# Kernel tuning notes

Measured on AMD Instinct MI355X. Metric: run time of the kernel, lower is better.

Reference implementation:

```python
import jax, jax.numpy as jnp
import numpy as np

N_WORDS, MAX_CHARS = 16384, 16
CE, H1, WE, H2 = 32, 64, 64, 128
CHAR_VOCAB, WORD_VOCAB, N_TAGS = 128, 50257, 64


def setup_inputs() -> dict:
    key = jax.random.key(0)
    ks = jax.random.split(key, 16)
    f = lambda k, shape: (jax.random.normal(k, shape, dtype=jnp.float32) * 0.1)
    return {
        "char_ids": jax.random.randint(ks[0], (N_WORDS, MAX_CHARS), 0, CHAR_VOCAB, dtype=jnp.int32),
        "word_ids": jax.random.randint(ks[1], (N_WORDS,), 0, WORD_VOCAB, dtype=jnp.int32),
        "char_lens": jax.random.randint(ks[2], (N_WORDS,), 1, MAX_CHARS + 1, dtype=jnp.int32),
        "char_emb": f(ks[3], (CHAR_VOCAB, CE)),
        "word_emb": f(ks[4], (WORD_VOCAB, WE)),
        "Wih1": f(ks[5], (4 * H1, CE)), "Whh1": f(ks[6], (4 * H1, H1)),
        "bih1": f(ks[7], (4 * H1,)), "bhh1": f(ks[8], (4 * H1,)),
        "Wih2": f(ks[9], (4 * H2, WE + H1)), "Whh2": f(ks[10], (4 * H2, H2)),
        "bih2": f(ks[11], (4 * H2,)), "bhh2": f(ks[12], (4 * H2,)),
        "Wtag": f(ks[13], (N_TAGS, H2)), "btag": f(ks[14], (N_TAGS,)),
    }


def _gates(pre, c, h_dim):
    i, fg, g, o = jnp.split(pre, 4, axis=-1)  # PyTorch LSTM gate order: i,f,g,o
    c_new = jax.nn.sigmoid(fg) * c + jax.nn.sigmoid(i) * jnp.tanh(g)
    h_new = jax.nn.sigmoid(o) * jnp.tanh(c_new)
    return h_new, c_new


def reference(char_ids, word_ids, char_lens, char_emb, word_emb,
              Wih1, Whh1, bih1, bhh1, Wih2, Whh2, bih2, bhh2, Wtag, btag):
    n_words, max_chars = char_ids.shape
    # ---- char LSTM, batched over all words, zero init per word ----
    cx = char_emb[char_ids]                      # [N, T, CE]
    cx = jnp.transpose(cx, (1, 0, 2))            # [T, N, CE]
    valid = (jnp.arange(max_chars)[:, None] < char_lens[None, :])  # [T, N]
    b1 = bih1 + bhh1

    def char_step(carry, inp):
        h, c = carry
        x, v = inp
        pre = x @ Wih1.T + h @ Whh1.T + b1
        h_new, c_new = _gates(pre, c, H1)
        v = v[:, None]
        return (jnp.where(v, h_new, h), jnp.where(v, c_new, c)), None

    h0 = jnp.zeros((n_words, Wih1.shape[0] // 4), cx.dtype)
    (h_char, _), _ = jax.lax.scan(char_step, (h0, h0), (cx, valid))  # h at true length

    # ---- word LSTM, sequential over words (hidden2 carried across) ----
    wx = jnp.concatenate([word_emb[word_ids], h_char], axis=-1)  # [N, WE+H1]
    b2 = bih2 + bhh2

    def word_step(carry, x):
        h, c = carry
        pre = x @ Wih2.T + h @ Whh2.T + b2
        h_new, c_new = _gates(pre, c, H2)
        return (h_new, c_new), h_new

    h20 = jnp.zeros((Wih2.shape[0] // 4,), wx.dtype)
    _, hs = jax.lax.scan(word_step, (h20, h20), wx)  # [N, H2]

    logits = hs @ Wtag.T + btag
    return jax.nn.log_softmax(logits, axis=1)
```

## Files before the change

### kernel.cpp

```cpp
#include <hip/hip_runtime.h>
#include <math.h>

#define N_WORDS 16384
#define MAX_CHARS 16
#define CE 32
#define H1 64
#define WE 64
#define H2 128
#define N_TAGS 64

typedef _Float16 f16x8 __attribute__((ext_vector_type(8)));
typedef float f32x4 __attribute__((ext_vector_type(4)));
typedef int i32x8 __attribute__((ext_vector_type(8)));

__device__ __forceinline__ float rcpf(float x) { return __builtin_amdgcn_rcpf(x); }
__device__ __forceinline__ float sigf(float x) { return rcpf(1.0f + __expf(-x)); }
__device__ __forceinline__ float tanh2(float x) {
    return 1.f - 2.f * rcpf(__expf(2.f * x) + 1.f);
}

extern "C" __global__ void __launch_bounds__(1024)
char_lstm_kernel(const int* __restrict__ char_ids, const int* __restrict__ char_lens,
                 const float* __restrict__ char_emb,
                 const float* __restrict__ Wih1, const float* __restrict__ Whh1,
                 const float* __restrict__ bih1, const float* __restrict__ bhh1,
                 float* __restrict__ h_char)
{
    extern __shared__ float lds[];
    float* Wc = lds;
    float* b1 = Wc + 256 * 97;
    float* xh = b1 + 256;
    const int tid = threadIdx.x;

    for (int idx = tid; idx < 256 * 96; idx += 1024) {
        int r = idx / 96, k = idx - r * 96;
        float v = (k < CE) ? Wih1[r * CE + k] : Whh1[r * H1 + (k - CE)];
        Wc[r * 97 + k] = v;
    }
    for (int r = tid; r < 256; r += 1024) b1[r] = bih1[r] + bhh1[r];
    __syncthreads();

    const int wlocal = tid >> 6;
    const int lane   = tid & 63;
    const int word   = blockIdx.x * 16 + wlocal;
    const int len    = char_lens[word];
    float h = 0.f, c = 0.f;
    float* xhw = xh + wlocal * 97;

    for (int t = 0; t < MAX_CHARS; ++t) {
        int cid = char_ids[word * MAX_CHARS + t];
        if (lane < CE) xhw[lane] = char_emb[cid * CE + lane];
        xhw[CE + lane] = h;
        __syncthreads();

        float a0 = 0.f, a1 = 0.f, a2 = 0.f, a3 = 0.f;
        const float* w0 = Wc + (0 * 64 + lane) * 97;
        const float* w1 = Wc + (1 * 64 + lane) * 97;
        const float* w2 = Wc + (2 * 64 + lane) * 97;
        const float* w3 = Wc + (3 * 64 + lane) * 97;
        #pragma unroll 8
        for (int k = 0; k < 96; ++k) {
            float x = xhw[k];
            a0 += w0[k] * x; a1 += w1[k] * x; a2 += w2[k] * x; a3 += w3[k] * x;
        }
        float pi = a0 + b1[lane];
        float pf = a1 + b1[64 + lane];
        float pg = a2 + b1[128 + lane];
        float po = a3 + b1[192 + lane];
        if (t < len) {
            float ig = sigf(pi), fg = sigf(pf), gg = tanh2(pg), og = sigf(po);
            c = fg * c + ig * gg;
            h = og * tanh2(c);
        }
        __syncthreads();
    }
    h_char[word * H1 + lane] = h;
}

extern "C" __global__ void __launch_bounds__(256)
xpre_gemm_kernel(const int* __restrict__ word_ids, const float* __restrict__ word_emb,
                 const float* __restrict__ h_char,
                 const float* __restrict__ Wih2,
                 const float* __restrict__ bih2, const float* __restrict__ bhh2,
                 float* __restrict__ xpre)
{
    __shared__ float Wl[64 * 130];
    __shared__ float Xl[32 * 130];
    const int tid = threadIdx.x;
    const int wb = blockIdx.x * 32;
    const int cb = blockIdx.y * 64;

    for (int idx = tid; idx < 64 * 128; idx += 256) {
        int r = idx >> 7, k = idx & 127;
        Wl[r * 130 + k] = Wih2[(cb + r) * H2 + k];
    }
    for (int idx = tid; idx < 32 * 128; idx += 256) {
        int w = idx >> 7, k = idx & 127;
        float v = (k < WE) ? word_emb[(long)word_ids[wb + w] * WE + k]
                           : h_char[(long)(wb + w) * H1 + (k - WE)];
        Xl[w * 130 + k] = v;
    }
    __syncthreads();

    const int tc = tid & 31;
    const int wg = tid >> 5;
    float acc[4][2] = {};
    for (int k = 0; k < 128; ++k) {
        float wv0 = Wl[tc * 130 + k];
        float wv1 = Wl[(tc + 32) * 130 + k];
        #pragma unroll
        for (int i = 0; i < 4; ++i) {
            float x = Xl[(wg * 4 + i) * 130 + k];
            acc[i][0] += x * wv0;
            acc[i][1] += x * wv1;
        }
    }
    int c0 = cb + tc, c1 = cb + tc + 32;
    float b0 = bih2[c0] + bhh2[c0];
    float b1v = bih2[c1] + bhh2[c1];
    int o0 = (c0 & 127) * 4 + (c0 >> 7);
    int o1 = (c1 & 127) * 4 + (c1 >> 7);
    #pragma unroll
    for (int i = 0; i < 4; ++i) {
        long w = wb + wg * 4 + i;
        xpre[w * 512 + o0] = acc[i][0] + b0;
        xpre[w * 512 + o1] = acc[i][1] + b1v;
    }
}

extern "C" __global__ void __launch_bounds__(512)
word_lstm_kernel(const float* __restrict__ xpre, const float* __restrict__ Whh2,
                 float* __restrict__ hs)
{
    __shared__ __align__(16) unsigned char h8[2][128];
    const int tid = threadIdx.x;
    const int w   = tid >> 6;
    const int l   = tid & 63;
    const int lg  = l >> 4;
    const int lc  = l & 15;
    const int hidx = 16 * w + lc;
    const bool writer = (l < 16);

    i32x8 af8[4];
    #pragma unroll
    for (int g = 0; g < 4; ++g) {
        const float* wrow = Whh2 + (size_t)(g * 128 + hidx) * 128 + lg * 32;
        i32x8 a;
        #pragma unroll
        for (int r = 0; r < 8; ++r) {
            int pk = __builtin_amdgcn_cvt_pk_fp8_f32(wrow[r * 4 + 0], wrow[r * 4 + 1], 0, false);
            pk = __builtin_amdgcn_cvt_pk_fp8_f32(wrow[r * 4 + 2], wrow[r * 4 + 3], pk, true);
            a[r] = pk;
        }
        af8[g] = a;
    }
    if (tid < 128) h8[0][tid] = 0;
    float c = 0.f;
    float4 xp = *(const float4*)(xpre + hidx * 4);
    float hbuf[8];
    const f32x4 zf = {0.f, 0.f, 0.f, 0.f};
    __syncthreads();

    for (int t8 = 0; t8 < N_WORDS / 8; ++t8) {
        #pragma unroll
        for (int j = 0; j < 8; ++j) {
            const int t = t8 * 8 + j;
            const int tn = (t + 1) & (N_WORDS - 1);
            float4 xpn = *(const float4*)(xpre + (size_t)tn * 512 + hidx * 4);

            const unsigned char* hb = h8[j & 1] + lg * 32;
            i32x8 bf = *(const i32x8*)hb;

            f32x4 acc[4];
            #pragma unroll
            for (int g = 0; g < 4; ++g)
                acc[g] = __builtin_amdgcn_mfma_scale_f32_16x16x128_f8f6f4(
                    bf, af8[g], zf, 0, 0, 0, 0x7F7F7F7F, 0, 0x7F7F7F7F);

            float p0 = acc[0][0] + xp.x;
            float p1 = acc[1][0] + xp.y;
            float p2 = acc[2][0] + xp.z;
            float p3 = acc[3][0] + xp.w;
            float ig = sigf(p0), fg = sigf(p1);
            float gg = tanh2(p2), og = sigf(p3);
            c = fg * c + ig * gg;
            float hn = og * tanh2(c);
            hbuf[j] = hn;
            if (writer) {
                int hp = __builtin_amdgcn_cvt_pk_fp8_f32(hn, hn, 0, false);
                h8[(j + 1) & 1][hidx] = (unsigned char)hp;
            }
            xp = xpn;

            asm volatile("s_waitcnt lgkmcnt(0)" ::: "memory");
            __builtin_amdgcn_sched_barrier(0);
            __builtin_amdgcn_s_barrier();
            __builtin_amdgcn_sched_barrier(0);
        }
        if (writer) {
            #pragma unroll
            for (int jj = 0; jj < 8; ++jj)
                hs[(size_t)(t8 * 8 + jj) * 128 + hidx] = hbuf[jj];
        }
    }
}

extern "C" __global__ void __launch_bounds__(256)
tag_kernel(const float* __restrict__ hs, const float* __restrict__ Wtag,
           const float* __restrict__ btag, float* __restrict__ out)
{
    __shared__ float Wl[64 * 129];
    const int tid = threadIdx.x;
    for (int idx = tid; idx < 64 * 128; idx += 256) {
        int r = idx >> 7, k = idx & 127;
        Wl[r * 129 + k] = Wtag[r * H2 + k];
    }
    __syncthreads();

    const int lane = tid & 63;
    const int word = blockIdx.x * 4 + (tid >> 6);
    const float* hrow = hs + (long)word * H2;
    float acc = btag[lane];
    #pragma unroll 4
    for (int k = 0; k < 128; ++k) acc += Wl[lane * 129 + k] * hrow[k];

    float m = acc;
    #pragma unroll
    for (int off = 32; off > 0; off >>= 1) m = fmaxf(m, __shfl_xor(m, off));
    float e = expf(acc - m);
    float s = e;
    #pragma unroll
    for (int off = 32; off > 0; off >>= 1) s += __shfl_xor(s, off);
    out[(long)word * N_TAGS + lane] = acc - m - logf(s);
}

extern "C" void kernel_launch(void* const* d_in, const int* in_sizes, int n_in,
                              void* d_out, int out_size, void* d_ws, size_t ws_size,
                              hipStream_t stream)
{
    (void)in_sizes; (void)n_in; (void)out_size; (void)ws_size;
    const int*   char_ids  = (const int*)d_in[0];
    const int*   word_ids  = (const int*)d_in[1];
    const int*   char_lens = (const int*)d_in[2];
    const float* char_emb  = (const float*)d_in[3];
    const float* word_emb  = (const float*)d_in[4];
    const float* Wih1 = (const float*)d_in[5];
    const float* Whh1 = (const float*)d_in[6];
    const float* bih1 = (const float*)d_in[7];
    const float* bhh1 = (const float*)d_in[8];
    const float* Wih2 = (const float*)d_in[9];
    const float* Whh2 = (const float*)d_in[10];
    const float* bih2 = (const float*)d_in[11];
    const float* bhh2 = (const float*)d_in[12];
    const float* Wtag = (const float*)d_in[13];
    const float* btag = (const float*)d_in[14];
    float* out = (float*)d_out;

    float* h_char = (float*)d_ws;
    float* xpre   = h_char + (size_t)N_WORDS * H1;
    float* hs     = xpre + (size_t)N_WORDS * 512;

    const int k1_lds = (256 * 97 + 256 + 16 * 97) * 4;
    hipFuncSetAttribute((const void*)char_lstm_kernel,
                        hipFuncAttributeMaxDynamicSharedMemorySize, k1_lds);

    char_lstm_kernel<<<N_WORDS / 16, 1024, k1_lds, stream>>>(
        char_ids, char_lens, char_emb, Wih1, Whh1, bih1, bhh1, h_char);

    dim3 g2(N_WORDS / 32, 8);
    xpre_gemm_kernel<<<g2, 256, 0, stream>>>(
        word_ids, word_emb, h_char, Wih2, bih2, bhh2, xpre);

    word_lstm_kernel<<<1, 512, 0, stream>>>(xpre, Whh2, hs);

    tag_kernel<<<N_WORDS / 4, 256, 0, stream>>>(hs, Wtag, btag, out);
}
```

Measured before the change: 6.369 ms.

## Move char LSTM to fp16 MFMA and prescale gates by log2e

Rewrites the char LSTM to hold fp16 weights in registers and run the gate GEMMs with 16x16x32 MFMA, using a small LDS double buffer for h. A prep kernel converts and reorders the weights, char embeddings and biases. All gate pre-activations are prescaled by log2(e) so sigmoid and tanh can call hardware exp2 directly. In the word LSTM the xpre bias is folded into the MFMA accumulator input. This trades fp32 accuracy for fp16 in the char LSTM and cuts scalar FMA and LDS traffic. The word LSTM, which is a sequential chain, likely dominates total time, so the overall effect may be modest.

```diff
diff --git a/kernel.cpp b/kernel.cpp
--- a/kernel.cpp
+++ b/kernel.cpp
@@ -8,73 +8,114 @@
 #define WE 64
 #define H2 128
 #define N_TAGS 64
+#define LOG2E 1.44269504f
+#define TWO_LOG2E 2.88539008f
 
 typedef _Float16 f16x8 __attribute__((ext_vector_type(8)));
 typedef float f32x4 __attribute__((ext_vector_type(4)));
 typedef int i32x8 __attribute__((ext_vector_type(8)));
 
 __device__ __forceinline__ float rcpf(float x) { return __builtin_amdgcn_rcpf(x); }
-__device__ __forceinline__ float sigf(float x) { return rcpf(1.0f + __expf(-x)); }
-__device__ __forceinline__ float tanh2(float x) {
-    return 1.f - 2.f * rcpf(__expf(2.f * x) + 1.f);
-}
-
-extern "C" __global__ void __launch_bounds__(1024)
-char_lstm_kernel(const int* __restrict__ char_ids, const int* __restrict__ char_lens,
-                 const float* __restrict__ char_emb,
-                 const float* __restrict__ Wih1, const float* __restrict__ Whh1,
-                 const float* __restrict__ bih1, const float* __restrict__ bhh1,
-                 float* __restrict__ h_char)
-{
-    extern __shared__ float lds[];
-    float* Wc = lds;
-    float* b1 = Wc + 256 * 97;
-    float* xh = b1 + 256;
-    const int tid = threadIdx.x;
-
-    for (int idx = tid; idx < 256 * 96; idx += 1024) {
+__device__ __forceinline__ float exp2f_hw(float x) { return __builtin_amdgcn_exp2f(x); }
+__device__ __forceinline__ float sig2(float p) { return rcpf(1.0f + exp2f_hw(-p)); }
+__device__ __forceinline__ float tanh2s(float p) {
+    return 1.f - 2.f * rcpf(exp2f_hw(2.f * p) + 1.f);
+}
+__device__ __forceinline__ float tanhc(float c) {
+    return 1.f - 2.f * rcpf(exp2f_hw(TWO_LOG2E * c) + 1.f);
+}
+
+extern "C" __global__ void __launch_bounds__(256)
+prep_kernel(const float* __restrict__ Wih1, const float* __restrict__ Whh1,
+            const float* __restrict__ bih1, const float* __restrict__ bhh1,
+            const float* __restrict__ char_emb,
+            _Float16* __restrict__ W16, _Float16* __restrict__ ce16,
+            float* __restrict__ b1s)
+{
+    int idx = blockIdx.x * 256 + threadIdx.x;
+    if (idx < 256 * 96) {
         int r = idx / 96, k = idx - r * 96;
         float v = (k < CE) ? Wih1[r * CE + k] : Whh1[r * H1 + (k - CE)];
-        Wc[r * 97 + k] = v;
-    }
-    for (int r = tid; r < 256; r += 1024) b1[r] = bih1[r] + bhh1[r];
+        W16[idx] = (_Float16)(v * LOG2E);
+    }
+    if (idx < 128 * 32) ce16[idx] = (_Float16)char_emb[idx];
+    if (idx < 256) b1s[idx] = (bih1[idx] + bhh1[idx]) * LOG2E;
+}
+
+extern "C" __global__ void __launch_bounds__(256)
+char_lstm_kernel(const int* __restrict__ char_ids, const int* __restrict__ char_lens,
+                 const _Float16* __restrict__ W16, const _Float16* __restrict__ ce16,
+                 const float* __restrict__ b1s, float* __restrict__ h_char)
+{
+    __shared__ _Float16 hl[2][16 * 72];
+    const int tid = threadIdx.x;
+    const int w  = tid >> 6;
+    const int l  = tid & 63;
+    const int lg = l >> 4;
+    const int lc = l & 15;
+    const int wb = blockIdx.x * 16;
+
+    f16x8 bfr[4][3];
+    #pragma unroll
+    for (int gt = 0; gt < 4; ++gt)
+        #pragma unroll
+        for (int kc = 0; kc < 3; ++kc)
+            bfr[gt][kc] = *(const f16x8*)(W16 + (size_t)(gt * 64 + 16 * w + lc) * 96
+                                          + kc * 32 + lg * 8);
+    float bb[4];
+    #pragma unroll
+    for (int gt = 0; gt < 4; ++gt) bb[gt] = b1s[gt * 64 + 16 * w + lc];
+
+    int cids[16];
+    {
+        const int4* cp = (const int4*)(char_ids + (size_t)(wb + lc) * 16);
+        #pragma unroll
+        for (int i = 0; i < 4; ++i) {
+            int4 v = cp[i];
+            cids[i * 4 + 0] = v.x; cids[i * 4 + 1] = v.y;
+            cids[i * 4 + 2] = v.z; cids[i * 4 + 3] = v.w;
+        }
+    }
+    int4 len4 = *(const int4*)(char_lens + wb + lg * 4);
+    int lens[4] = {len4.x, len4.y, len4.z, len4.w};
+
+    float hreg[4] = {0.f, 0.f, 0.f, 0.f};
+    float creg[4] = {0.f, 0.f, 0.f, 0.f};
+    for (int i = tid; i < 16 * 72; i += 256) hl[0][i] = (_Float16)0.f;
     __syncthreads();
 
-    const int wlocal = tid >> 6;
-    const int lane   = tid & 63;
-    const int word   = blockIdx.x * 16 + wlocal;
-    const int len    = char_lens[word];
-    float h = 0.f, c = 0.f;
-    float* xhw = xh + wlocal * 97;
-
+    #pragma unroll
     for (int t = 0; t < MAX_CHARS; ++t) {
-        int cid = char_ids[word * MAX_CHARS + t];
-        if (lane < CE) xhw[lane] = char_emb[cid * CE + lane];
-        xhw[CE + lane] = h;
+        const _Float16* hb = hl[t & 1];
+        f16x8 ax  = *(const f16x8*)(ce16 + (size_t)cids[t] * 32 + lg * 8);
+        f16x8 ah1 = *(const f16x8*)(hb + lc * 72 + lg * 8);
+        f16x8 ah2 = *(const f16x8*)(hb + lc * 72 + 32 + lg * 8);
+        f32x4 acc[4];
+        #pragma unroll
+        for (int gt = 0; gt < 4; ++gt) {
+            f32x4 cb = {bb[gt], bb[gt], bb[gt], bb[gt]};
+            acc[gt] = __builtin_amdgcn_mfma_f32_16x16x32_f16(ax,  bfr[gt][0], cb, 0, 0, 0);
+            acc[gt] = __builtin_amdgcn_mfma_f32_16x16x32_f16(ah1, bfr[gt][1], acc[gt], 0, 0, 0);
+            acc[gt] = __builtin_amdgcn_mfma_f32_16x16x32_f16(ah2, bfr[gt][2], acc[gt], 0, 0, 0);
+        }
+        #pragma unroll
+        for (int q = 0; q < 4; ++q) {
+            float ig = sig2(acc[0][q]);
+            float fg = sig2(acc[1][q]);
+            float gg = tanh2s(acc[2][q]);
+            float og = sig2(acc[3][q]);
+            float cn = fg * creg[q] + ig * gg;
+            float hn = og * tanhc(cn);
+            bool v = t < lens[q];
+            creg[q] = v ? cn : creg[q];
+            hreg[q] = v ? hn : hreg[q];
+            hl[(t + 1) & 1][(lg * 4 + q) * 72 + 16 * w + lc] = (_Float16)hreg[q];
+        }
         __syncthreads();
-
-        float a0 = 0.f, a1 = 0.f, a2 = 0.f, a3 = 0.f;
-        const float* w0 = Wc + (0 * 64 + lane) * 97;
-        const float* w1 = Wc + (1 * 64 + lane) * 97;
-        const float* w2 = Wc + (2 * 64 + lane) * 97;
-        const float* w3 = Wc + (3 * 64 + lane) * 97;
-        #pragma unroll 8
-        for (int k = 0; k < 96; ++k) {
-            float x = xhw[k];
-            a0 += w0[k] * x; a1 += w1[k] * x; a2 += w2[k] * x; a3 += w3[k] * x;
-        }
-        float pi = a0 + b1[lane];
-        float pf = a1 + b1[64 + lane];
-        float pg = a2 + b1[128 + lane];
-        float po = a3 + b1[192 + lane];
-        if (t < len) {
-            float ig = sigf(pi), fg = sigf(pf), gg = tanh2(pg), og = sigf(po);
-            c = fg * c + ig * gg;
-            h = og * tanh2(c);
-        }
-        __syncthreads();
-    }
-    h_char[word * H1 + lane] = h;
+    }
+    #pragma unroll
+    for (int q = 0; q < 4; ++q)
+        h_char[(size_t)(wb + lg * 4 + q) * H1 + 16 * w + lc] = hreg[q];
 }
 
 extern "C" __global__ void __launch_bounds__(256)
@@ -123,8 +164,8 @@
     #pragma unroll
     for (int i = 0; i < 4; ++i) {
         long w = wb + wg * 4 + i;
-        xpre[w * 512 + o0] = acc[i][0] + b0;
-        xpre[w * 512 + o1] = acc[i][1] + b1v;
+        xpre[w * 512 + o0] = (acc[i][0] + b0) * LOG2E;
+        xpre[w * 512 + o1] = (acc[i][1] + b1v) * LOG2E;
     }
 }
 
@@ -148,8 +189,10 @@
         i32x8 a;
         #pragma unroll
         for (int r = 0; r < 8; ++r) {
-            int pk = __builtin_amdgcn_cvt_pk_fp8_f32(wrow[r * 4 + 0], wrow[r * 4 + 1], 0, false);
-            pk = __builtin_amdgcn_cvt_pk_fp8_f32(wrow[r * 4 + 2], wrow[r * 4 + 3], pk, true);
+            int pk = __builtin_amdgcn_cvt_pk_fp8_f32(
+                wrow[r * 4 + 0] * LOG2E, wrow[r * 4 + 1] * LOG2E, 0, false);
+            pk = __builtin_amdgcn_cvt_pk_fp8_f32(
+                wrow[r * 4 + 2] * LOG2E, wrow[r * 4 + 3] * LOG2E, pk, true);
             a[r] = pk;
         }
         af8[g] = a;
@@ -158,7 +201,6 @@
     float c = 0.f;
     float4 xp = *(const float4*)(xpre + hidx * 4);
     float hbuf[8];
-    const f32x4 zf = {0.f, 0.f, 0.f, 0.f};
     __syncthreads();
 
     for (int t8 = 0; t8 < N_WORDS / 8; ++t8) {
@@ -173,18 +215,19 @@
 
             f32x4 acc[4];
             #pragma unroll
-            for (int g = 0; g < 4; ++g)
+            for (int g = 0; g < 4; ++g) {
+                float xg = (g == 0) ? xp.x : (g == 1) ? xp.y : (g == 2) ? xp.z : xp.w;
+                f32x4 cxp = {xg, xg, xg, xg};
                 acc[g] = __builtin_amdgcn_mfma_scale_f32_16x16x128_f8f6f4(
-                    bf, af8[g], zf, 0, 0, 0, 0x7F7F7F7F, 0, 0x7F7F7F7F);
-
-            float p0 = acc[0][0] + xp.x;
-            float p1 = acc[1][0] + xp.y;
-            float p2 = acc[2][0] + xp.z;
-            float p3 = acc[3][0] + xp.w;
-            float ig = sigf(p0), fg = sigf(p1);
-            float gg = tanh2(p2), og = sigf(p3);
+                    bf, af8[g], cxp, 0, 0, 0, 0x7F7F7F7F, 0, 0x7F7F7F7F);
+            }
+
+            float ig = sig2(acc[0][0]);
+            float fg = sig2(acc[1][0]);
+            float gg = tanh2s(acc[2][0]);
+            float og = sig2(acc[3][0]);
             c = fg * c + ig * gg;
-            float hn = og * tanh2(c);
+            float hn = og * tanhc(c);
             hbuf[j] = hn;
             if (writer) {
                 int hp = __builtin_amdgcn_cvt_pk_fp8_f32(hn, hn, 0, false);
@@ -259,13 +302,15 @@
     float* h_char = (float*)d_ws;
     float* xpre   = h_char + (size_t)N_WORDS * H1;
     float* hs     = xpre + (size_t)N_WORDS * 512;
-
-    const int k1_lds = (256 * 97 + 256 + 16 * 97) * 4;
-    hipFuncSetAttribute((const void*)char_lstm_kernel,
-                        hipFuncAttributeMaxDynamicSharedMemorySize, k1_lds);
-
-    char_lstm_kernel<<<N_WORDS / 16, 1024, k1_lds, stream>>>(
-        char_ids, char_lens, char_emb, Wih1, Whh1, bih1, bhh1, h_char);
+    _Float16* W16  = (_Float16*)hs;
+    _Float16* ce16 = W16 + 256 * 96;
+    float*    b1s  = (float*)(ce16 + 128 * 32);
+
+    prep_kernel<<<96, 256, 0, stream>>>(Wih1, Whh1, bih1, bhh1, char_emb,
+                                        W16, ce16, b1s);
+
+    char_lstm_kernel<<<N_WORDS / 16, 256, 0, stream>>>(
+        char_ids, char_lens, W16, ce16, b1s, h_char);
 
     dim3 g2(N_WORDS / 32, 8);
     xpre_gemm_kernel<<<g2, 256, 0, stream>>>(
```

Measured after the change: 6.280 ms. Within noise of the previous version (-1.4%).
